# Performance work log

Hardware: AMD Instinct MI355X
Metric: run time of the kernel (lower is better)

The kernel has to match this reference:

```python
import jax, jax.numpy as jnp
import numpy as np

EPS = 1e-5  # BatchNorm2d default eps


def _resize_bilinear(x, out_h, out_w):
    # PyTorch F.interpolate(mode='bilinear', align_corners=False, antialias=False):
    # input coord = (out + 0.5)/scale - 0.5  ->  translation = 0.5*(scale-1)
    b, c, h, w = x.shape
    sh, sw = out_h / h, out_w / w
    scale = jnp.array([sh, sw], dtype=jnp.float32)
    trans = jnp.array([0.5 * (sh - 1.0), 0.5 * (sw - 1.0)], dtype=jnp.float32)
    return jax.image.scale_and_translate(
        x, (b, c, out_h, out_w), (2, 3), scale, trans,
        method='linear', antialias=False)


def setup_inputs() -> dict:
    key = jax.random.key(0)
    ks = jax.random.split(key, 6)
    B, C, IC, H, W = 4, 64, 16, 128, 128
    init = lambda k, shape, fan_in: (
        jax.random.normal(k, shape, jnp.float32) / np.float32(np.sqrt(fan_in)))
    return {
        'x': jax.random.normal(ks[0], (B, C, H, W), jnp.float32),
        'g_w': init(ks[1], (IC, C), C), 'g_b': jnp.zeros((IC,), jnp.float32),
        'theta_w': init(ks[2], (IC, C), C), 'theta_b': jnp.zeros((IC,), jnp.float32),
        'phi_w': init(ks[3], (IC, C), C), 'phi_b': jnp.zeros((IC,), jnp.float32),
        'out_w': init(ks[4], (C, IC), IC), 'out_b': jnp.zeros((C,), jnp.float32),
        'bn_gamma': jnp.ones((C,), jnp.float32), 'bn_beta': jnp.zeros((C,), jnp.float32),
    }


def reference(x, g_w, g_b, theta_w, theta_b, phi_w, phi_b,
              out_w, out_b, bn_gamma, bn_beta):
    b, c, h, w = x.shape
    dh, dw = h // 2, w // 2          # downsample_factor = 0.5
    xd = _resize_bilinear(x, dh, dw).reshape(b, c, dh * dw)  # [b,C,N]

    # 1x1 convs == per-pixel linear projections
    g_x = jnp.einsum('bcn,oc->bno', xd, g_w) + g_b          # [b,N,IC]
    th = jnp.einsum('bcn,oc->bno', xd, theta_w) + theta_b   # [b,N,IC]
    ph = jnp.einsum('bcn,oc->bon', xd, phi_w) + phi_b[None, :, None]  # [b,IC,N]

    f = jnp.einsum('bni,bim->bnm', th, ph)   # [b,N,N] score matrix (no scaling)
    attn = jax.nn.softmax(f, axis=-1)
    y = jnp.einsum('bnm,bmi->bni', attn, g_x)               # [b,N,IC]
    y = y.transpose(0, 2, 1).reshape(b, -1, dh, dw)         # [b,IC,dh,dw]

    y = _resize_bilinear(y, h, w)                            # upsample back
    y = jnp.einsum('bihw,ci->bchw', y, out_w) + out_b[None, :, None, None]

    z = x + y
    # BatchNorm2d in (default) training mode: biased batch stats over (B,H,W)
    mean = jnp.mean(z, axis=(0, 2, 3))
    var = jnp.var(z, axis=(0, 2, 3))
    zn = (z - mean[None, :, None, None]) * jax.lax.rsqrt(var + EPS)[None, :, None, None]
    return zn * bn_gamma[None, :, None, None] + bn_beta[None, :, None, None]
```

## Files before the change

kernel.cpp:

```cpp
#include <hip/hip_runtime.h>
#include <math.h>

#define NB 4
#define NC 64
#define NI 16
#define NH 128
#define NW 128
#define ND 64
#define NN 4096
#define KSPL 4

#define LOG2E 1.4426950408889634f

using bfrag  = __attribute__((ext_vector_type(8))) short;
using bfrag4 = __attribute__((ext_vector_type(4))) short;
using ffrag  = __attribute__((ext_vector_type(4))) float;

#if __has_builtin(__builtin_amdgcn_exp2f)
#define EXP2(x) __builtin_amdgcn_exp2f(x)
#else
#define EXP2(x) exp2f(x)
#endif

__device__ __forceinline__ unsigned bf16rne(float f) {
    unsigned u = __float_as_uint(f);
    return (u + 0x7FFFu + ((u >> 16) & 1u)) >> 16;
}
__device__ __forceinline__ unsigned pk_rne(float lo, float hi) {
    return bf16rne(lo) | (bf16rne(hi) << 16);
}
__device__ __forceinline__ unsigned pk_trunc(float lo, float hi) {
    return (__float_as_uint(lo) >> 16) | (__float_as_uint(hi) & 0xFFFF0000u);
}

__device__ __forceinline__ ffrag mfma_qk(bfrag4 a, bfrag4 b, ffrag c) {
#if __has_builtin(__builtin_amdgcn_mfma_f32_16x16x16bf16_1k)
    return __builtin_amdgcn_mfma_f32_16x16x16bf16_1k(a, b, c, 0, 0, 0);
#else
    union { bfrag4 h[2]; bfrag v; } ua, ub;
    bfrag4 zz = {0, 0, 0, 0};
    ua.h[0] = a; ua.h[1] = zz;
    ub.h[0] = b; ub.h[1] = zz;
    return __builtin_amdgcn_mfma_f32_16x16x32_bf16(ua.v, ub.v, c, 0, 0, 0);
#endif
}

extern "C" __global__ __launch_bounds__(256)
void k_proj(const float* __restrict__ x,
            const float* __restrict__ gw, const float* __restrict__ gb,
            const float* __restrict__ tw, const float* __restrict__ tb,
            const float* __restrict__ pw, const float* __restrict__ pb,
            uint2* __restrict__ th_sw, uint2* __restrict__ phi_sw,
            uint4* __restrict__ g_sw, float* __restrict__ shstats)
{
    __shared__ float swt[NC][48];
    __shared__ float sb[48];
    __shared__ float red[3][64][49];
    __shared__ __align__(16) unsigned short gtile[16][64];
    int tid = threadIdx.x;
    int b = blockIdx.x >> 6, i = blockIdx.x & 63;
    if (blockIdx.x == 0) {
#pragma unroll
        for (int k = 0; k < 4; ++k) shstats[tid + k*256] = 0.f;
    }
    for (int idx = tid; idx < NI*NC; idx += 256) {
        int o = idx >> 6, c = idx & 63;
        swt[c][o]      = tw[idx];
        swt[c][16 + o] = pw[idx];
        swt[c][32 + o] = gw[idx];
    }
    if (tid < 16) { sb[tid] = tb[tid]; sb[16+tid] = pb[tid]; sb[32+tid] = gb[tid]; }
    __syncthreads();

    int j = tid & 63, part = tid >> 6;
    const float* xp = x + (((size_t)(b*NC + part*16))*NH + (2*i+1))*NW + (2*j+1);
    float a[48];
#pragma unroll
    for (int k = 0; k < 48; ++k) a[k] = 0.f;
    for (int cc = 0; cc < 16; ++cc) {
        float xd = xp[(size_t)cc*NH*NW];
        const float* wr = swt[part*16 + cc];
#pragma unroll
        for (int k = 0; k < 48; ++k) a[k] += xd*wr[k];
    }
    if (part != 0) {
#pragma unroll
        for (int k = 0; k < 48; ++k) red[part-1][j][k] = a[k];
    }
    __syncthreads();
    if (part == 0) {
        float aT[16], aP[16], aG[16];
#pragma unroll
        for (int o = 0; o < 16; ++o) {
            float vT = a[o]    + red[0][j][o]    + red[1][j][o]    + red[2][j][o];
            float vP = a[16+o] + red[0][j][16+o] + red[1][j][16+o] + red[2][j][16+o];
            float vG = a[32+o] + red[0][j][32+o] + red[1][j][32+o] + red[2][j][32+o];
            aT[o] = (vT + sb[o]) * LOG2E;
            aP[o] =  vP + sb[16+o];
            aG[o] =  vG + sb[32+o];
        }
        int q = i*64 + j;
        int n = j & 15;
        size_t qtile = (size_t)b*256 + (q >> 4);
#pragma unroll
        for (int qd = 0; qd < 4; ++qd)
            th_sw[qtile*64 + qd*16 + n] =
                make_uint2(pk_rne(aT[4*qd], aT[4*qd+1]), pk_rne(aT[4*qd+2], aT[4*qd+3]));
        int wk = j & 31;
        int f = (wk >> 2) & 1;
        int r = ((wk >> 3) << 2) | (wk & 3);
        size_t kgrp = (size_t)b*256 + (q >> 5)*2 + f;
#pragma unroll
        for (int qd = 0; qd < 4; ++qd)
            phi_sw[kgrp*64 + qd*16 + r] =
                make_uint2(pk_rne(aP[4*qd], aP[4*qd+1]), pk_rne(aP[4*qd+2], aP[4*qd+3]));
#pragma unroll
        for (int o = 0; o < 16; ++o) gtile[o][j] = (unsigned short)bf16rne(aG[o]);
    }
    __syncthreads();
    if (tid < 128) {
        int c2 = tid >> 6, L = tid & 63;
        int n = L & 15, q8 = L >> 4;
        const uint4* src = (const uint4*)&gtile[n][c2*32 + q8*8];
        g_sw[((size_t)b*128 + i*2 + c2)*64 + L] = *src;
    }
}

extern "C" __global__ __launch_bounds__(256, 4)
void k_attn(const uint2* __restrict__ th_sw, const uint2* __restrict__ phi_sw,
            const uint4* __restrict__ g_sw, float* __restrict__ accp,
            float* __restrict__ lp)
{
    __shared__ __align__(16) uint2 sphi[16*64];
    __shared__ __align__(16) uint4 sg[8*64];
    int tid = threadIdx.x;
    int wave = tid >> 6, lane = tid & 63;
    int quad = lane >> 4, low = lane & 15;
    int qgroup = blockIdx.x, ks = blockIdx.y, b = blockIdx.z;

    union { uint2 u; bfrag4 f; } thu;
    thu.u = th_sw[((size_t)b*256 + qgroup*4 + wave)*64 + lane];
    bfrag4 theta = thu.f;

    ffrag yacc = {0.f, 0.f, 0.f, 0.f};
    const ffrag zf = {0.f, 0.f, 0.f, 0.f};
    float lacc = 0.f;

    for (int chunk = 0; chunk < 4; ++chunk) {
        __syncthreads();
        const uint4* srcP = (const uint4*)(phi_sw + ((size_t)b*256 + ks*64 + chunk*16)*64);
        const uint4* srcG = g_sw + ((size_t)b*128 + ks*32 + chunk*8)*64;
        ((uint4*)sphi)[tid]       = srcP[tid];
        ((uint4*)sphi)[256 + tid] = srcP[256 + tid];
        sg[tid]       = srcG[tid];
        sg[256 + tid] = srcG[256 + tid];
        __syncthreads();

        const bfrag4* sphiF = (const bfrag4*)sphi;
        const bfrag*  sgF   = (const bfrag*)sg;
#pragma unroll
        for (int s = 0; s < 8; ++s) {
            bfrag4 pA = sphiF[(2*s+0)*64 + lane];
            bfrag4 pB = sphiF[(2*s+1)*64 + lane];
            bfrag  vf = sgF[s*64 + lane];
            ffrag sA = mfma_qk(pA, theta, zf);
            ffrag sB = mfma_qk(pB, theta, zf);
            float eA0 = EXP2(sA[0]), eA1 = EXP2(sA[1]), eA2 = EXP2(sA[2]), eA3 = EXP2(sA[3]);
            float eB0 = EXP2(sB[0]), eB1 = EXP2(sB[1]), eB2 = EXP2(sB[2]), eB3 = EXP2(sB[3]);
            lacc += ((eA0+eA1) + (eA2+eA3)) + ((eB0+eB1) + (eB2+eB3));
            union { unsigned u[4]; bfrag f; } pu;
            pu.u[0] = pk_trunc(eA0, eA1);
            pu.u[1] = pk_trunc(eA2, eA3);
            pu.u[2] = pk_trunc(eB0, eB1);
            pu.u[3] = pk_trunc(eB2, eB3);
            yacc = __builtin_amdgcn_mfma_f32_16x16x32_bf16(pu.f, vf, yacc, 0, 0, 0);
        }
    }

    lacc += __shfl_xor(lacc, 16, 64);
    lacc += __shfl_xor(lacc, 32, 64);

    int qbase = qgroup*64 + wave*16;
    size_t pbase = ((size_t)ks*NB + b)*NN;
#pragma unroll
    for (int reg = 0; reg < 4; ++reg)
        accp[(pbase + qbase + quad*4 + reg)*16 + low] = yacc[reg];
    if (lane < 16) lp[pbase + qbase + lane] = lacc;
}

extern "C" __global__ __launch_bounds__(256)
void k_outz(const float* __restrict__ accp, const float* __restrict__ lp,
            const float* __restrict__ x, const float* __restrict__ ow,
            const float* __restrict__ ob, float* __restrict__ z,
            float* __restrict__ shstats)
{
    __shared__ float slab[16*257];
    __shared__ float syd[2][NI][ND];
    __shared__ float sl[2][ND];
    __shared__ float swv[NC*NI];
    __shared__ float sbv[NC];
    int t = threadIdx.x;
    int hp = blockIdx.x, b = blockIdx.y;
    for (int idx = t; idx < NC*NI; idx += 256) swv[idx] = ow[idx];
    if (t < NC) sbv[t] = ob[t];

    {
        int r = t >> 7, col = (t >> 1) & 63, half = t & 1;
        int row = (r == 0) ? (hp > 0 ? hp-1 : 0) : hp;
        int q = row*64 + col;
        float4 a0 = make_float4(0.f,0.f,0.f,0.f), a1 = a0;
        float lsum = 0.f;
        for (int ks = 0; ks < KSPL; ++ks) {
            const float4* ap = (const float4*)accp + (((size_t)ks*NB + b)*NN + q)*4 + 2*half;
            float4 v0 = ap[0], v1 = ap[1];
            a0.x += v0.x; a0.y += v0.y; a0.z += v0.z; a0.w += v0.w;
            a1.x += v1.x; a1.y += v1.y; a1.z += v1.z; a1.w += v1.w;
            if (half == 0) lsum += lp[((size_t)ks*NB + b)*NN + q];
        }
        if (half == 0) sl[r][col] = lsum;
        __syncthreads();
        float inv = 1.f / sl[r][col];
        int i0 = 8*half;
        syd[r][i0+0][col] = a0.x*inv; syd[r][i0+1][col] = a0.y*inv;
        syd[r][i0+2][col] = a0.z*inv; syd[r][i0+3][col] = a0.w*inv;
        syd[r][i0+4][col] = a1.x*inv; syd[r][i0+5][col] = a1.y*inv;
        syd[r][i0+6][col] = a1.z*inv; syd[r][i0+7][col] = a1.w*inv;
    }
    __syncthreads();

    int w = t & 127, hsel = t >> 7;
    int h = 2*hp + hsel;
    float wh0 = hsel ? 0.f : 0.5f;
    float wh1 = hsel ? 1.f : 0.5f;
    int c0, c1; float wc0, wc1;
    if (w & 1) { c0 = c1 = (w-1) >> 1; wc0 = 1.f; wc1 = 0.f; }
    else       { c1 = w >> 1; c0 = c1 ? c1-1 : 0; wc0 = 0.5f; wc1 = 0.5f; }
    float yv[16];
#pragma unroll
    for (int i = 0; i < 16; ++i)
        yv[i] = wh0*(wc0*syd[0][i][c0] + wc1*syd[0][i][c1])
              + wh1*(wc0*syd[1][i][c0] + wc1*syd[1][i][c1]);

    const float* xb = x + (((size_t)(b*NC))*NH + h)*NW + w;
    float* zb       = z + (((size_t)(b*NC))*NH + h)*NW + w;
    float* shadow = shstats + ((((unsigned)b << 6) + (unsigned)hp) & 7u)*128;
    int ch = t >> 4, idx = t & 15;

    for (int ck = 0; ck < 4; ++ck) {
        __syncthreads();
#pragma unroll
        for (int cc = 0; cc < 16; ++cc) {
            int c = ck*16 + cc;
            const float* wr = swv + c*16;
            float acc = sbv[c];
#pragma unroll
            for (int i = 0; i < 16; ++i) acc += wr[i]*yv[i];
            float zv = xb[(size_t)c*NH*NW] + acc;
            zb[(size_t)c*NH*NW] = zv;
            slab[cc*257 + t] = zv;
        }
        __syncthreads();
        float s = 0.f, s2 = 0.f;
#pragma unroll
        for (int k = 0; k < 16; ++k) {
            int p = idx*16 + ((k + idx) & 15);
            float v = slab[ch*257 + p];
            s += v; s2 += v*v;
        }
        s  += __shfl_xor(s, 1);  s  += __shfl_xor(s, 2);
        s  += __shfl_xor(s, 4);  s  += __shfl_xor(s, 8);
        s2 += __shfl_xor(s2, 1); s2 += __shfl_xor(s2, 2);
        s2 += __shfl_xor(s2, 4); s2 += __shfl_xor(s2, 8);
        if (idx == 0) atomicAdd(shadow + ck*16 + ch, s);
        if (idx == 1) atomicAdd(shadow + 64 + ck*16 + ch, s2);
    }
}

extern "C" __global__ __launch_bounds__(256)
void k_norm(const float* __restrict__ z, const float* __restrict__ shstats,
            const float* __restrict__ gamma, const float* __restrict__ beta,
            float* __restrict__ out)
{
    __shared__ float sga[NC], sbe[NC];
    int t = threadIdx.x;
    if (t < NC) {
        float s = 0.f, s2 = 0.f;
#pragma unroll
        for (int sh = 0; sh < 8; ++sh) {
            s  += shstats[sh*128 + t];
            s2 += shstats[sh*128 + 64 + t];
        }
        const float inv_cnt = 1.f/65536.f;
        float mean = s*inv_cnt;
        float var  = s2*inv_cnt - mean*mean;
        float rs = rsqrtf(var + 1e-5f);
        float ga = gamma[t]*rs;
        sga[t] = ga;
        sbe[t] = beta[t] - mean*ga;
    }
    __syncthreads();
#pragma unroll
    for (int it = 0; it < 4; ++it) {
        size_t i4 = ((size_t)blockIdx.x*4 + it)*256 + t;
        int c = (int)((i4 >> 12) & 63);
        float4 v = ((const float4*)z)[i4];
        float ga = sga[c], be = sbe[c];
        ((float4*)out)[i4] = make_float4(v.x*ga+be, v.y*ga+be, v.z*ga+be, v.w*ga+be);
    }
}

extern "C" void kernel_launch(void* const* d_in, const int* in_sizes, int n_in,
                              void* d_out, int out_size, void* d_ws, size_t ws_size,
                              hipStream_t stream)
{
    const float* x     = (const float*)d_in[0];
    const float* gw    = (const float*)d_in[1];
    const float* gb    = (const float*)d_in[2];
    const float* tw    = (const float*)d_in[3];
    const float* tb    = (const float*)d_in[4];
    const float* pw    = (const float*)d_in[5];
    const float* pb    = (const float*)d_in[6];
    const float* ow    = (const float*)d_in[7];
    const float* ob    = (const float*)d_in[8];
    const float* gamma = (const float*)d_in[9];
    const float* beta  = (const float*)d_in[10];
    float* out = (float*)d_out;

    char* wsb = (char*)d_ws;
    uint2* th_sw  = (uint2*)(wsb);
    uint2* phi_sw = (uint2*)(wsb + (512u<<10));
    uint4* g_sw   = (uint4*)(wsb + (1024u<<10));
    float* lp     = (float*)(wsb + (1536u<<10));
    float* shst   = (float*)(wsb + (1792u<<10));
    float* accp   = (float*)(wsb + (2048u<<10));
    float* z      = (float*)(wsb + (6u<<20) + (256u<<10));

    k_proj<<<256, 256, 0, stream>>>(x, gw, gb, tw, tb, pw, pb,
                                    th_sw, phi_sw, g_sw, shst);
    k_attn<<<dim3(64, KSPL, NB), 256, 0, stream>>>(th_sw, phi_sw, g_sw, accp, lp);
    k_outz<<<dim3(64, NB), 256, 0, stream>>>(accp, lp, x, ow, ob, z, shst);
    k_norm<<<1024, 256, 0, stream>>>(z, shst, gamma, beta, out);
}
```

Measured before the change: 128.8 us.

## Compute theta/phi/g projections with bf16 MFMA instead of scalar FMA

Rewrites the projection kernel to stage the strided downsampled x row into shared memory, pack weights into bf16 MFMA fragments, and compute the three 16-channel 1x1 projections with 16x16x32 bf16 MFMA instructions. This replaces the per-thread 48-accumulator scalar FMA loop and the cross-wave shared-memory reduction. It adds bf16 rounding of x and the weights before accumulation, which changes numerics slightly, and depends on the fragment layouts matching what the attention kernel expects.

```diff
diff --git a/kernel.cpp b/kernel.cpp
--- a/kernel.cpp
+++ b/kernel.cpp
@@ -53,9 +53,9 @@
             uint2* __restrict__ th_sw, uint2* __restrict__ phi_sw,
             uint4* __restrict__ g_sw, float* __restrict__ shstats)
 {
-    __shared__ float swt[NC][48];
-    __shared__ float sb[48];
-    __shared__ float red[3][64][49];
+    __shared__ __align__(16) uint4 wfrag[6*64];
+    __shared__ __align__(16) float sbias[48];
+    __shared__ __align__(16) float xstage[64*68];
     __shared__ __align__(16) unsigned short gtile[16][64];
     int tid = threadIdx.x;
     int b = blockIdx.x >> 6, i = blockIdx.x & 63;
@@ -63,59 +63,76 @@
 #pragma unroll
         for (int k = 0; k < 4; ++k) shstats[tid + k*256] = 0.f;
     }
-    for (int idx = tid; idx < NI*NC; idx += 256) {
-        int o = idx >> 6, c = idx & 63;
-        swt[c][o]      = tw[idx];
-        swt[c][16 + o] = pw[idx];
-        swt[c][32 + o] = gw[idx];
-    }
-    if (tid < 16) { sb[tid] = tb[tid]; sb[16+tid] = pb[tid]; sb[32+tid] = gb[tid]; }
+
+    for (int idx = tid; idx < 384; idx += 256) {
+        int t = idx / 128, kh = (idx >> 6) & 1, L = idx & 63;
+        int quad = L >> 4, m = L & 15;
+        int c0 = kh*32 + quad*8;
+        const float* src = (t == 0) ? tw : (t == 1) ? pw : gw;
+        const float4* s4 = (const float4*)(src + m*64 + c0);
+        float4 w0 = s4[0], w1 = s4[1];
+        wfrag[idx] = make_uint4(pk_rne(w0.x, w0.y), pk_rne(w0.z, w0.w),
+                                pk_rne(w1.x, w1.y), pk_rne(w1.z, w1.w));
+    }
+    if (tid < 16) { sbias[tid] = tb[tid]; sbias[16+tid] = pb[tid]; sbias[32+tid] = gb[tid]; }
+
+    {
+        int c = tid >> 2, seg = tid & 3;
+        const float* xr = x + (((size_t)(b*NC + c))*NH + (2*i+1))*NW + 1;
+#pragma unroll
+        for (int p = 0; p < 16; ++p) {
+            int jx = seg*16 + p;
+            xstage[jx*68 + c] = xr[2*jx];
+        }
+    }
     __syncthreads();
 
-    int j = tid & 63, part = tid >> 6;
-    const float* xp = x + (((size_t)(b*NC + part*16))*NH + (2*i+1))*NW + (2*j+1);
-    float a[48];
-#pragma unroll
-    for (int k = 0; k < 48; ++k) a[k] = 0.f;
-    for (int cc = 0; cc < 16; ++cc) {
-        float xd = xp[(size_t)cc*NH*NW];
-        const float* wr = swt[part*16 + cc];
-#pragma unroll
-        for (int k = 0; k < 48; ++k) a[k] += xd*wr[k];
-    }
-    if (part != 0) {
-#pragma unroll
-        for (int k = 0; k < 48; ++k) red[part-1][j][k] = a[k];
-    }
-    __syncthreads();
-    if (part == 0) {
-        float aT[16], aP[16], aG[16];
-#pragma unroll
-        for (int o = 0; o < 16; ++o) {
-            float vT = a[o]    + red[0][j][o]    + red[1][j][o]    + red[2][j][o];
-            float vP = a[16+o] + red[0][j][16+o] + red[1][j][16+o] + red[2][j][16+o];
-            float vG = a[32+o] + red[0][j][32+o] + red[1][j][32+o] + red[2][j][32+o];
-            aT[o] = (vT + sb[o]) * LOG2E;
-            aP[o] =  vP + sb[16+o];
-            aG[o] =  vG + sb[32+o];
-        }
-        int q = i*64 + j;
-        int n = j & 15;
-        size_t qtile = (size_t)b*256 + (q >> 4);
-#pragma unroll
-        for (int qd = 0; qd < 4; ++qd)
-            th_sw[qtile*64 + qd*16 + n] =
-                make_uint2(pk_rne(aT[4*qd], aT[4*qd+1]), pk_rne(aT[4*qd+2], aT[4*qd+3]));
-        int wk = j & 31;
-        int f = (wk >> 2) & 1;
-        int r = ((wk >> 3) << 2) | (wk & 3);
-        size_t kgrp = (size_t)b*256 + (q >> 5)*2 + f;
-#pragma unroll
-        for (int qd = 0; qd < 4; ++qd)
-            phi_sw[kgrp*64 + qd*16 + r] =
-                make_uint2(pk_rne(aP[4*qd], aP[4*qd+1]), pk_rne(aP[4*qd+2], aP[4*qd+3]));
-#pragma unroll
-        for (int o = 0; o < 16; ++o) gtile[o][j] = (unsigned short)bf16rne(aG[o]);
+    int wave = tid >> 6, lane = tid & 63;
+    int quad = lane >> 4, low = lane & 15;
+
+    union { uint4 u; bfrag f; } xb0, xb1;
+    {
+        const float4* row = (const float4*)(xstage + (wave*16 + low)*68);
+        float4 a0 = row[quad*2 + 0], a1 = row[quad*2 + 1];
+        float4 b0 = row[8 + quad*2 + 0], b1 = row[8 + quad*2 + 1];
+        xb0.u = make_uint4(pk_rne(a0.x,a0.y), pk_rne(a0.z,a0.w),
+                           pk_rne(a1.x,a1.y), pk_rne(a1.z,a1.w));
+        xb1.u = make_uint4(pk_rne(b0.x,b0.y), pk_rne(b0.z,b0.w),
+                           pk_rne(b1.x,b1.y), pk_rne(b1.z,b1.w));
+    }
+
+    const ffrag zf = {0.f, 0.f, 0.f, 0.f};
+    const bfrag* wfF = (const bfrag*)wfrag;
+    {
+        ffrag acc = __builtin_amdgcn_mfma_f32_16x16x32_bf16(wfF[0*64+lane], xb0.f, zf, 0,0,0);
+        acc = __builtin_amdgcn_mfma_f32_16x16x32_bf16(wfF[1*64+lane], xb1.f, acc, 0,0,0);
+        float4 bias4 = *(const float4*)&sbias[quad*4];
+        float v0 = (acc[0]+bias4.x)*LOG2E, v1 = (acc[1]+bias4.y)*LOG2E;
+        float v2 = (acc[2]+bias4.z)*LOG2E, v3 = (acc[3]+bias4.w)*LOG2E;
+        th_sw[((size_t)b*256 + i*4 + wave)*64 + lane] =
+            make_uint2(pk_rne(v0, v1), pk_rne(v2, v3));
+    }
+    {
+        ffrag acc = __builtin_amdgcn_mfma_f32_16x16x32_bf16(wfF[2*64+lane], xb0.f, zf, 0,0,0);
+        acc = __builtin_amdgcn_mfma_f32_16x16x32_bf16(wfF[3*64+lane], xb1.f, acc, 0,0,0);
+        float4 bias4 = *(const float4*)&sbias[16 + quad*4];
+        float v0 = acc[0]+bias4.x, v1 = acc[1]+bias4.y;
+        float v2 = acc[2]+bias4.z, v3 = acc[3]+bias4.w;
+        int w32 = (wave & 1)*16 + low;
+        int f = (w32 >> 2) & 1;
+        int rr = ((w32 >> 3) << 2) | (w32 & 3);
+        size_t kgrp = (size_t)b*256 + (i*2 + (wave >> 1))*2 + f;
+        phi_sw[kgrp*64 + quad*16 + rr] = make_uint2(pk_rne(v0, v1), pk_rne(v2, v3));
+    }
+    {
+        ffrag acc = __builtin_amdgcn_mfma_f32_16x16x32_bf16(wfF[4*64+lane], xb0.f, zf, 0,0,0);
+        acc = __builtin_amdgcn_mfma_f32_16x16x32_bf16(wfF[5*64+lane], xb1.f, acc, 0,0,0);
+        float4 bias4 = *(const float4*)&sbias[32 + quad*4];
+#pragma unroll
+        for (int r = 0; r < 4; ++r) {
+            float bv = (r==0)?bias4.x:(r==1)?bias4.y:(r==2)?bias4.z:bias4.w;
+            gtile[quad*4 + r][wave*16 + low] = (unsigned short)bf16rne(acc[r] + bv);
+        }
     }
     __syncthreads();
     if (tid < 128) {
```

Result: faster. 124.8 us (-3.2%).
